# Performance work log

Hardware: AMD Instinct MI355X
Metric: run time of the kernel (lower is better)

## Reference

```python
import jax, jax.numpy as jnp
import numpy as np

ROPE_BASE = 10000.0
WINDOW = 1024  # per_layer_sliding_window
SCALE = 0.08838834764831845  # 1/sqrt(128)
NEG_INF = -1e30


def _apply_rope(x, positions):
    # x: [B, S, H, D]; positions: [B, S] int
    D = x.shape[-1]
    inv_freq = 1.0 / (ROPE_BASE ** (jnp.arange(0, D, 2, dtype=jnp.float32) / D))  # [D/2]
    ang = positions.astype(jnp.float32)[..., None] * inv_freq          # [B, S, D/2]
    cos = jnp.cos(ang)[:, :, None, :]                                   # [B, S, 1, D/2]
    sin = jnp.sin(ang)[:, :, None, :]
    x1, x2 = x[..., : D // 2], x[..., D // 2 :]
    return jnp.concatenate([x1 * cos - x2 * sin, x2 * cos + x1 * sin], axis=-1)


def setup_inputs() -> dict:
    key = jax.random.key(0)
    k1, k2, k3, k4 = jax.random.split(key, 4)
    B, S, H, KV, D = 1, 2048, 32, 8, 128
    q = jax.random.normal(k1, (B, S, H, D), dtype=jnp.float32)
    k = jax.random.normal(k2, (B, S, KV, D), dtype=jnp.float32)
    v = jax.random.normal(k3, (B, S, KV, D), dtype=jnp.float32)
    positions = jnp.broadcast_to(jnp.arange(S, dtype=jnp.int32), (B, S))
    sinks = jax.random.normal(k4, (H,), dtype=jnp.float32)
    return {"q": q, "k": k, "v": v, "positions": positions, "sinks": sinks}


def reference(q, k, v, positions, sinks):
    # q: [B,S,H,D]; k,v: [B,S,KV,D]; positions: [B,S]; sinks: [H]
    B, S, H, D = q.shape
    KV = k.shape[2]
    group = H // KV

    qr = _apply_rope(q, positions)
    kr = _apply_rope(k, positions)

    # GQA: expand kv heads to match q heads
    kr = jnp.repeat(kr, group, axis=2)  # [B,S,H,D]
    ve = jnp.repeat(v, group, axis=2)   # [B,S,H,D]

    scores = jnp.einsum("bqhd,bkhd->bhqk", qr, kr) * SCALE  # [B,H,Q,K]

    pq = positions[:, :, None]  # [B,Q,1]
    pk = positions[:, None, :]  # [B,1,K]
    allowed = (pk <= pq) & (pq - pk < WINDOW)               # causal + sliding window
    scores = jnp.where(allowed[:, None, :, :], scores, NEG_INF)

    # softmax with per-head attention sink logit in the denominator
    sink = sinks[None, :, None]                             # [1,H,1]
    m = jnp.maximum(jnp.max(scores, axis=-1), sink)         # [B,H,Q]
    p = jnp.exp(scores - m[..., None])                      # [B,H,Q,K]
    denom = jnp.sum(p, axis=-1) + jnp.exp(sink - m)         # [B,H,Q]
    out = jnp.einsum("bhqk,bkhd->bqhd", p, ve) / denom.transpose(0, 2, 1)[..., None]
    return out  # [B,S,H,D]
```

## Files before the change

### kernel.cpp

```cpp
#include <hip/hip_runtime.h>

#define S_LEN 2048
#define NH 32
#define NKV 8
#define HD 128
#define WINDOW 1024
#define SCALEF 0.08838834764831845f
#define NEG_INF_F -1e30f
#define NEG_L2_10K_O64 -0.2076205059304601f
#define LOG2E 1.442695040888963f
#define CSHIFT_L2 17.31234049067355f

typedef unsigned short ushort_t;
typedef __attribute__((ext_vector_type(8))) short short8;
typedef __attribute__((ext_vector_type(4))) float floatx4;
typedef __attribute__((ext_vector_type(4))) int intx4;

static __device__ __forceinline__ float fexp2(float x) {
  return __builtin_amdgcn_exp2f(x);
}

static __device__ __forceinline__ ushort_t f2bf(float f) {
  union { float f; unsigned u; } un; un.f = f;
  unsigned r = un.u + 0x7fffu + ((un.u >> 16) & 1u);
  return (ushort_t)(r >> 16);
}

static __device__ __forceinline__ unsigned pack2bf(float a, float b) {
  return (unsigned)f2bf(a) | ((unsigned)f2bf(b) << 16);
}

__device__ __forceinline__ void gl_lds16(const ushort_t* g, ushort_t* l) {
  __builtin_amdgcn_global_load_lds(
      (const __attribute__((address_space(1))) unsigned int*)g,
      (__attribute__((address_space(3))) unsigned int*)l, 16, 0, 0);
}

__global__ __launch_bounds__(256) void prep_kv(
    const float* __restrict__ k, const float* __restrict__ v,
    const int* __restrict__ positions, ushort_t* __restrict__ Kr,
    ushort_t* __restrict__ Vt) {
  __shared__ float lv[64][129];
  const int kv = blockIdx.x & 7;
  const int s0 = (blockIdx.x >> 3) * 64;
  const int tid = threadIdx.x;

  {
    const int i = tid & 63;
    const int wrow = tid >> 6;
    const float invf = fexp2((float)i * NEG_L2_10K_O64);
#pragma unroll 4
    for (int it = 0; it < 16; ++it) {
      int s = s0 + it * 4 + wrow;
      float pos = (float)positions[s];
      const float* kp = k + ((size_t)s * NKV + kv) * HD;
      float x1 = kp[i], x2 = kp[i + 64];
      float sn, cs;
      __sincosf(pos * invf, &sn, &cs);
      ushort_t* o = Kr + ((size_t)kv * S_LEN + s) * HD;
      o[i] = f2bf(x1 * cs - x2 * sn);
      o[i + 64] = f2bf(x2 * cs + x1 * sn);
    }
  }
  {
    const int d = tid & 127;
    const int r2 = tid >> 7;
#pragma unroll
    for (int it = 0; it < 32; ++it) {
      int row = it * 2 + r2;
      lv[row][d] = v[((size_t)(s0 + row) * NKV + kv) * HD + d];
    }
  }
  __syncthreads();
  {
    const int ss = tid & 63;
    const int d0 = tid >> 6;
#pragma unroll
    for (int it = 0; it < 32; ++it) {
      int d = d0 + it * 4;
      Vt[((size_t)kv * HD + d) * S_LEN + s0 + ss] = f2bf(lv[ss][d]);
    }
  }
}

__global__ __launch_bounds__(256, 4) void attn_kernel(
    const float* __restrict__ q, const int* __restrict__ positions,
    const float* __restrict__ sinks, const ushort_t* __restrict__ Kr,
    const ushort_t* __restrict__ Vt, float* __restrict__ out) {
  __shared__ __align__(16) ushort_t smem[16384];

  const int tid = threadIdx.x;
  const int w = tid >> 6;
  const int lane = tid & 63;
  const int quad = lane >> 4;
  const int l16 = lane & 15;
  const int kv = blockIdx.x & 7;
  const int tile = blockIdx.x >> 3;
  const int h = kv * 4 + w;
  const int q0 = tile * 16;

  ushort_t* Qsw = smem + w * 2048;
  {
    const float invf = fexp2((float)lane * NEG_L2_10K_O64);
#pragma unroll 4
    for (int row = 0; row < 16; ++row) {
      float pos = (float)positions[q0 + row];
      const float* qp = q + ((size_t)(q0 + row) * NH + h) * HD;
      float x1 = qp[lane], x2 = qp[lane + 64];
      float sn, cs;
      __sincosf(pos * invf, &sn, &cs);
      float o1 = (x1 * cs - x2 * sn) * SCALEF;
      float o2 = (x2 * cs + x1 * sn) * SCALEF;
      int c1_ = (lane >> 3) ^ row;
      int c2_ = ((lane >> 3) + 8) ^ row;
      Qsw[row * 128 + c1_ * 8 + (lane & 7)] = f2bf(o1);
      Qsw[row * 128 + c2_ * 8 + (lane & 7)] = f2bf(o2);
    }
  }
  short8 qf[4];
#pragma unroll
  for (int t = 0; t < 4; ++t)
    qf[t] = *(const short8*)&Qsw[l16 * 128 + (((4 * t + quad) ^ l16) * 8)];
  __syncthreads();

  const ushort_t* KrH = Kr + (size_t)kv * S_LEN * HD;
  const ushort_t* VtH = Vt + (size_t)kv * HD * S_LEN;
  int kgo[2], vgo[2], ldst[2];
#pragma unroll
  for (int i = 0; i < 2; ++i) {
    int slot = i * 256 + tid;
    int key = slot >> 4;
    int cin = (slot & 15) ^ (key & 15);
    kgo[i] = key * HD + cin * 8;
    int d = slot >> 2;
    int qcin = (slot & 3) ^ ((d ^ (d >> 2)) & 3);
    vgo[i] = d * S_LEN + qcin * 8;
    ldst[i] = (i * 256 + (tid & 192)) * 8;
  }

  auto stage = [&](int b, int koff) {
#pragma unroll
    for (int i = 0; i < 2; ++i) {
      gl_lds16(KrH + (size_t)koff * HD + kgo[i], smem + b * 4096 + ldst[i]);
      gl_lds16(VtH + koff + vgo[i], smem + 8192 + b * 4096 + ldst[i]);
    }
  };

  floatx4 O4[8];
#pragma unroll
  for (int i = 0; i < 8; ++i) O4[i] = (floatx4){0.f, 0.f, 0.f, 0.f};
  float lsum = 0.f;

  const int cbeg = (q0 > 1023) ? ((q0 - 1023) >> 5) : 0;
  const int cend = (q0 + 15) >> 5;

  stage(0, cbeg * 32);
  __syncthreads();

  for (int ci = cbeg; ci <= cend; ++ci) {
    const int b = (ci - cbeg) & 1;
    const int koff = ci * 32;
    if (ci < cend) stage(b ^ 1, koff + 32);

    const ushort_t* KsB = smem + b * 4096;
    const ushort_t* VsB = smem + 8192 + b * 4096;

    floatx4 s0v = (floatx4){0.f, 0.f, 0.f, 0.f};
    floatx4 s1v = (floatx4){0.f, 0.f, 0.f, 0.f};
#pragma unroll
    for (int t = 0; t < 4; ++t) {
      int ch = ((4 * t + quad) ^ l16) * 8;
      short8 k0 = *(const short8*)&KsB[l16 * 128 + ch];
      short8 k1 = *(const short8*)&KsB[(l16 + 16) * 128 + ch];
      s0v = __builtin_amdgcn_mfma_f32_16x16x32_bf16(k0, qf[t], s0v, 0, 0, 0);
      s1v = __builtin_amdgcn_mfma_f32_16x16x32_bf16(k1, qf[t], s1v, 0, 0, 0);
    }

    if (koff + 31 > q0 || koff < q0 - 1008) {
      const int qp_ = q0 + l16;
#pragma unroll
      for (int r = 0; r < 4; ++r) {
        int k0i = koff + quad * 4 + r, k1i = k0i + 16;
        if (!((k0i <= qp_) && (qp_ - k0i < WINDOW))) s0v[r] = NEG_INF_F;
        if (!((k1i <= qp_) && (qp_ - k1i < WINDOW))) s1v[r] = NEG_INF_F;
      }
    }

    float pc0[4], pc1[4];
#pragma unroll
    for (int r = 0; r < 4; ++r) {
      pc0[r] = fexp2(fmaf(s0v[r], LOG2E, -CSHIFT_L2));
      pc1[r] = fexp2(fmaf(s1v[r], LOG2E, -CSHIFT_L2));
    }
    lsum += (pc0[0] + pc0[1]) + (pc0[2] + pc0[3]) +
            (pc1[0] + pc1[1]) + (pc1[2] + pc1[3]);

    unsigned pk0[2] = {pack2bf(pc0[0], pc0[1]), pack2bf(pc0[2], pc0[3])};
    unsigned pk1[2] = {pack2bf(pc1[0], pc1[1]), pack2bf(pc1[2], pc1[3])};
    intx4 bi;
    const int sbase = ((quad & 1) * 2) * 16 + l16;
#pragma unroll
    for (int u = 0; u < 4; ++u) {
      int src = sbase + (u >> 1) * 16;
      int lo = __shfl((int)pk0[u & 1], src);
      int hi = __shfl((int)pk1[u & 1], src);
      bi[u] = (quad < 2) ? lo : hi;
    }
    short8 pb = __builtin_bit_cast(short8, bi);

#pragma unroll
    for (int i = 0; i < 8; ++i) {
      int d = 16 * i + l16;
      short8 vf = *(const short8*)&VsB[d * 32 + ((quad ^ ((d ^ (d >> 2)) & 3)) * 8)];
      O4[i] = __builtin_amdgcn_mfma_f32_16x16x32_bf16(vf, pb, O4[i], 0, 0, 0);
    }

    __syncthreads();
  }

  lsum += __shfl_xor(lsum, 16);
  lsum += __shfl_xor(lsum, 32);
  lsum += fexp2(fmaf(sinks[h], LOG2E, -CSHIFT_L2));
  const float rl = 1.0f / lsum;

  float* op = out + ((size_t)(q0 + l16) * NH + h) * HD;
#pragma unroll
  for (int i = 0; i < 8; ++i) {
    floatx4 val = O4[i] * rl;
    *(floatx4*)(op + 16 * i + quad * 4) = val;
  }
}

extern "C" void kernel_launch(void* const* d_in, const int* in_sizes, int n_in,
                              void* d_out, int out_size, void* d_ws, size_t ws_size,
                              hipStream_t stream) {
  const float* q = (const float*)d_in[0];
  const float* k = (const float*)d_in[1];
  const float* v = (const float*)d_in[2];
  const int* positions = (const int*)d_in[3];
  const float* sinks = (const float*)d_in[4];
  float* out = (float*)d_out;

  ushort_t* Kr = (ushort_t*)d_ws;
  ushort_t* Vt = Kr + (size_t)NKV * S_LEN * HD;

  prep_kv<<<NKV * (S_LEN / 64), 256, 0, stream>>>(k, v, positions, Kr, Vt);
  attn_kernel<<<NKV * (S_LEN / 16), 256, 0, stream>>>(q, positions, sinks, Kr, Vt, out);
}
```

Before: 148.5 us.

## Rewrite attention with 32x32 MFMA, fragment-ordered K/V layout, and split-K waves

The K and V preprocessing now writes rotated K and transposed V straight into MFMA fragment order, so the attention kernel loads operands from global memory into registers and no longer stages them through LDS. Each block handles two query heads per wave pair using 32x32x16 bf16 MFMA. The key chunks are split across two waves and their partial results are merged through LDS at the end. Query tiles are paired, one early and one late, to balance causal work across blocks, and the fixed exp shift is removed in favour of folding log2e into the Q scale. The risks are overflow, since exp is no longer shifted, more register pressure, and more global load latency without double buffering.

```diff
diff --git a/kernel.cpp b/kernel.cpp
--- a/kernel.cpp
+++ b/kernel.cpp
@@ -5,15 +5,14 @@
 #define NKV 8
 #define HD 128
 #define WINDOW 1024
-#define SCALEF 0.08838834764831845f
 #define NEG_INF_F -1e30f
 #define NEG_L2_10K_O64 -0.2076205059304601f
-#define LOG2E 1.442695040888963f
-#define CSHIFT_L2 17.31234049067355f
+#define LOG2E_F 1.442695040888963f
 
 typedef unsigned short ushort_t;
 typedef __attribute__((ext_vector_type(8))) short short8;
 typedef __attribute__((ext_vector_type(4))) float floatx4;
+typedef __attribute__((ext_vector_type(16))) float floatx16;
 typedef __attribute__((ext_vector_type(4))) int intx4;
 
 static __device__ __forceinline__ float fexp2(float x) {
@@ -26,21 +25,17 @@
   return (ushort_t)(r >> 16);
 }
 
-static __device__ __forceinline__ unsigned pack2bf(float a, float b) {
-  return (unsigned)f2bf(a) | ((unsigned)f2bf(b) << 16);
-}
-
-__device__ __forceinline__ void gl_lds16(const ushort_t* g, ushort_t* l) {
-  __builtin_amdgcn_global_load_lds(
-      (const __attribute__((address_space(1))) unsigned int*)g,
-      (__attribute__((address_space(3))) unsigned int*)l, 16, 0, 0);
+static __device__ __forceinline__ unsigned packP(float a, float b) {
+  unsigned ua = __builtin_bit_cast(unsigned, a) + 0x8000u;
+  unsigned ub = __builtin_bit_cast(unsigned, b) + 0x8000u;
+  return __builtin_amdgcn_perm(ub, ua, 0x07060302u);
 }
 
 __global__ __launch_bounds__(256) void prep_kv(
     const float* __restrict__ k, const float* __restrict__ v,
-    const int* __restrict__ positions, ushort_t* __restrict__ Kr,
-    ushort_t* __restrict__ Vt) {
-  __shared__ float lv[64][129];
+    const int* __restrict__ positions, ushort_t* __restrict__ Kr2,
+    ushort_t* __restrict__ Vt2) {
+  __shared__ __align__(16) ushort_t lt[64 * 136];
   const int kv = blockIdx.x & 7;
   const int s0 = (blockIdx.x >> 3) * 64;
   const int tid = threadIdx.x;
@@ -51,183 +46,218 @@
     const float invf = fexp2((float)i * NEG_L2_10K_O64);
 #pragma unroll 4
     for (int it = 0; it < 16; ++it) {
-      int s = s0 + it * 4 + wrow;
+      int row = it * 4 + wrow;
+      int s = s0 + row;
       float pos = (float)positions[s];
       const float* kp = k + ((size_t)s * NKV + kv) * HD;
       float x1 = kp[i], x2 = kp[i + 64];
       float sn, cs;
       __sincosf(pos * invf, &sn, &cs);
-      ushort_t* o = Kr + ((size_t)kv * S_LEN + s) * HD;
-      o[i] = f2bf(x1 * cs - x2 * sn);
-      o[i + 64] = f2bf(x2 * cs + x1 * sn);
-    }
-  }
+      lt[row * 136 + i] = f2bf(x1 * cs - x2 * sn);
+      lt[row * 136 + i + 64] = f2bf(x2 * cs + x1 * sn);
+    }
+  }
+  __syncthreads();
+#pragma unroll
+  for (int it = 0; it < 4; ++it) {
+    int slot = it * 256 + tid;
+    int kb_l = slot >> 9;
+    int rem = slot & 511;
+    int t = rem >> 6;
+    int lane = rem & 63;
+    int key_l = kb_l * 32 + (lane & 31);
+    int dbase = t * 16 + (lane >> 5) * 8;
+    short8 val = *(const short8*)&lt[key_l * 136 + dbase];
+    *(short8*)&Kr2[(size_t)(kv * 64 + (s0 >> 5) + kb_l) * 4096 + t * 512 + lane * 8] = val;
+  }
+  __syncthreads();
   {
     const int d = tid & 127;
     const int r2 = tid >> 7;
 #pragma unroll
     for (int it = 0; it < 32; ++it) {
       int row = it * 2 + r2;
-      lv[row][d] = v[((size_t)(s0 + row) * NKV + kv) * HD + d];
+      lt[row * 136 + d] = f2bf(v[((size_t)(s0 + row) * NKV + kv) * HD + d]);
     }
   }
   __syncthreads();
-  {
-    const int ss = tid & 63;
-    const int d0 = tid >> 6;
-#pragma unroll
-    for (int it = 0; it < 32; ++it) {
-      int d = d0 + it * 4;
-      Vt[((size_t)kv * HD + d) * S_LEN + s0 + ss] = f2bf(lv[ss][d]);
-    }
-  }
-}
-
-__global__ __launch_bounds__(256, 4) void attn_kernel(
+#pragma unroll
+  for (int it = 0; it < 4; ++it) {
+    int slot = it * 256 + tid;
+    int kh_l = slot >> 8;
+    int rem = slot & 255;
+    int tl = rem >> 6;
+    int lane = rem & 63;
+    int d = tl * 32 + (lane & 31);
+    int key0 = kh_l * 16 + (lane >> 5) * 8;
+    unsigned w0 = (unsigned)lt[(key0 + 0) * 136 + d] | ((unsigned)lt[(key0 + 1) * 136 + d] << 16);
+    unsigned w1 = (unsigned)lt[(key0 + 2) * 136 + d] | ((unsigned)lt[(key0 + 3) * 136 + d] << 16);
+    unsigned w2 = (unsigned)lt[(key0 + 4) * 136 + d] | ((unsigned)lt[(key0 + 5) * 136 + d] << 16);
+    unsigned w3 = (unsigned)lt[(key0 + 6) * 136 + d] | ((unsigned)lt[(key0 + 7) * 136 + d] << 16);
+    intx4 val = {(int)w0, (int)w1, (int)w2, (int)w3};
+    *(intx4*)&Vt2[(size_t)(kv * 128 + (s0 >> 4) + kh_l) * 2048 + tl * 512 + lane * 8] = val;
+  }
+}
+
+__global__ __launch_bounds__(256, 3) void attn_kernel(
     const float* __restrict__ q, const int* __restrict__ positions,
-    const float* __restrict__ sinks, const ushort_t* __restrict__ Kr,
-    const ushort_t* __restrict__ Vt, float* __restrict__ out) {
-  __shared__ __align__(16) ushort_t smem[16384];
+    const float* __restrict__ sinks, const ushort_t* __restrict__ Kr2,
+    const ushort_t* __restrict__ Vt2, float* __restrict__ out) {
+  __shared__ __align__(16) ushort_t smem[20480];
+  __shared__ float lsx[64];
 
   const int tid = threadIdx.x;
   const int w = tid >> 6;
   const int lane = tid & 63;
-  const int quad = lane >> 4;
-  const int l16 = lane & 15;
+  const int u = lane >> 5;
+  const int l15 = lane & 15;
+  const int hp = w & 1;
+  const int kw = w >> 1;
   const int kv = blockIdx.x & 7;
-  const int tile = blockIdx.x >> 3;
-  const int h = kv * 4 + w;
-  const int q0 = tile * 16;
-
-  ushort_t* Qsw = smem + w * 2048;
-  {
-    const float invf = fexp2((float)lane * NEG_L2_10K_O64);
+  const int bid = blockIdx.x >> 3;
+  const int h = kv * 4 + hp * 2 + ((lane >> 4) & 1);
+  const float QSCALE = (float)(0.08838834764831845 * 1.4426950408889634);
+
+  const ushort_t* KbL = Kr2 + (size_t)kv * 64 * 4096 + lane * 8;
+  const ushort_t* VbL = Vt2 + (size_t)kv * 128 * 2048 + lane * 8;
+
+  int tiles[2];
+  int ntiles;
+  if (bid < 64) { tiles[0] = bid + 64; tiles[1] = 0; ntiles = 1; }
+  else          { tiles[0] = bid - 64; tiles[1] = 127 - bid; ntiles = 2; }
+
+  for (int ti = 0; ti < ntiles; ++ti) {
+    const int q0 = tiles[ti] * 16;
+
+    {
+      const int hh = w;
+      const int rbase = (hh >> 1) * 4096;
+      const int i = lane;
+      const float invf = fexp2((float)i * NEG_L2_10K_O64);
+      const int t1 = i >> 4;
+      const int j = i & 7;
+      const int lhalf = ((i >> 3) & 1) * 32 + (hh & 1) * 16;
 #pragma unroll 4
-    for (int row = 0; row < 16; ++row) {
-      float pos = (float)positions[q0 + row];
-      const float* qp = q + ((size_t)(q0 + row) * NH + h) * HD;
-      float x1 = qp[lane], x2 = qp[lane + 64];
-      float sn, cs;
-      __sincosf(pos * invf, &sn, &cs);
-      float o1 = (x1 * cs - x2 * sn) * SCALEF;
-      float o2 = (x2 * cs + x1 * sn) * SCALEF;
-      int c1_ = (lane >> 3) ^ row;
-      int c2_ = ((lane >> 3) + 8) ^ row;
-      Qsw[row * 128 + c1_ * 8 + (lane & 7)] = f2bf(o1);
-      Qsw[row * 128 + c2_ * 8 + (lane & 7)] = f2bf(o2);
-    }
-  }
-  short8 qf[4];
-#pragma unroll
-  for (int t = 0; t < 4; ++t)
-    qf[t] = *(const short8*)&Qsw[l16 * 128 + (((4 * t + quad) ^ l16) * 8)];
-  __syncthreads();
-
-  const ushort_t* KrH = Kr + (size_t)kv * S_LEN * HD;
-  const ushort_t* VtH = Vt + (size_t)kv * HD * S_LEN;
-  int kgo[2], vgo[2], ldst[2];
-#pragma unroll
-  for (int i = 0; i < 2; ++i) {
-    int slot = i * 256 + tid;
-    int key = slot >> 4;
-    int cin = (slot & 15) ^ (key & 15);
-    kgo[i] = key * HD + cin * 8;
-    int d = slot >> 2;
-    int qcin = (slot & 3) ^ ((d ^ (d >> 2)) & 3);
-    vgo[i] = d * S_LEN + qcin * 8;
-    ldst[i] = (i * 256 + (tid & 192)) * 8;
-  }
-
-  auto stage = [&](int b, int koff) {
-#pragma unroll
-    for (int i = 0; i < 2; ++i) {
-      gl_lds16(KrH + (size_t)koff * HD + kgo[i], smem + b * 4096 + ldst[i]);
-      gl_lds16(VtH + koff + vgo[i], smem + 8192 + b * 4096 + ldst[i]);
-    }
-  };
-
-  floatx4 O4[8];
-#pragma unroll
-  for (int i = 0; i < 8; ++i) O4[i] = (floatx4){0.f, 0.f, 0.f, 0.f};
-  float lsum = 0.f;
-
-  const int cbeg = (q0 > 1023) ? ((q0 - 1023) >> 5) : 0;
-  const int cend = (q0 + 15) >> 5;
-
-  stage(0, cbeg * 32);
-  __syncthreads();
-
-  for (int ci = cbeg; ci <= cend; ++ci) {
-    const int b = (ci - cbeg) & 1;
-    const int koff = ci * 32;
-    if (ci < cend) stage(b ^ 1, koff + 32);
-
-    const ushort_t* KsB = smem + b * 4096;
-    const ushort_t* VsB = smem + 8192 + b * 4096;
-
-    floatx4 s0v = (floatx4){0.f, 0.f, 0.f, 0.f};
-    floatx4 s1v = (floatx4){0.f, 0.f, 0.f, 0.f};
-#pragma unroll
-    for (int t = 0; t < 4; ++t) {
-      int ch = ((4 * t + quad) ^ l16) * 8;
-      short8 k0 = *(const short8*)&KsB[l16 * 128 + ch];
-      short8 k1 = *(const short8*)&KsB[(l16 + 16) * 128 + ch];
-      s0v = __builtin_amdgcn_mfma_f32_16x16x32_bf16(k0, qf[t], s0v, 0, 0, 0);
-      s1v = __builtin_amdgcn_mfma_f32_16x16x32_bf16(k1, qf[t], s1v, 0, 0, 0);
-    }
-
-    if (koff + 31 > q0 || koff < q0 - 1008) {
-      const int qp_ = q0 + l16;
-#pragma unroll
-      for (int r = 0; r < 4; ++r) {
-        int k0i = koff + quad * 4 + r, k1i = k0i + 16;
-        if (!((k0i <= qp_) && (qp_ - k0i < WINDOW))) s0v[r] = NEG_INF_F;
-        if (!((k1i <= qp_) && (qp_ - k1i < WINDOW))) s1v[r] = NEG_INF_F;
-      }
-    }
-
-    float pc0[4], pc1[4];
-#pragma unroll
-    for (int r = 0; r < 4; ++r) {
-      pc0[r] = fexp2(fmaf(s0v[r], LOG2E, -CSHIFT_L2));
-      pc1[r] = fexp2(fmaf(s1v[r], LOG2E, -CSHIFT_L2));
-    }
-    lsum += (pc0[0] + pc0[1]) + (pc0[2] + pc0[3]) +
-            (pc1[0] + pc1[1]) + (pc1[2] + pc1[3]);
-
-    unsigned pk0[2] = {pack2bf(pc0[0], pc0[1]), pack2bf(pc0[2], pc0[3])};
-    unsigned pk1[2] = {pack2bf(pc1[0], pc1[1]), pack2bf(pc1[2], pc1[3])};
-    intx4 bi;
-    const int sbase = ((quad & 1) * 2) * 16 + l16;
-#pragma unroll
-    for (int u = 0; u < 4; ++u) {
-      int src = sbase + (u >> 1) * 16;
-      int lo = __shfl((int)pk0[u & 1], src);
-      int hi = __shfl((int)pk1[u & 1], src);
-      bi[u] = (quad < 2) ? lo : hi;
-    }
-    short8 pb = __builtin_bit_cast(short8, bi);
-
-#pragma unroll
-    for (int i = 0; i < 8; ++i) {
-      int d = 16 * i + l16;
-      short8 vf = *(const short8*)&VsB[d * 32 + ((quad ^ ((d ^ (d >> 2)) & 3)) * 8)];
-      O4[i] = __builtin_amdgcn_mfma_f32_16x16x32_bf16(vf, pb, O4[i], 0, 0, 0);
-    }
-
-    __syncthreads();
-  }
-
-  lsum += __shfl_xor(lsum, 16);
-  lsum += __shfl_xor(lsum, 32);
-  lsum += fexp2(fmaf(sinks[h], LOG2E, -CSHIFT_L2));
-  const float rl = 1.0f / lsum;
-
-  float* op = out + ((size_t)(q0 + l16) * NH + h) * HD;
-#pragma unroll
-  for (int i = 0; i < 8; ++i) {
-    floatx4 val = O4[i] * rl;
-    *(floatx4*)(op + 16 * i + quad * 4) = val;
+      for (int row = 0; row < 16; ++row) {
+        float pos = (float)positions[q0 + row];
+        const float* qp = q + ((size_t)(q0 + row) * NH + kv * 4 + hh) * HD;
+        float x1 = qp[i], x2 = qp[i + 64];
+        float sn, cs;
+        __sincosf(pos * invf, &sn, &cs);
+        int ldst = rbase + (lhalf + row) * 8 + j;
+        smem[ldst + t1 * 512] = f2bf((x1 * cs - x2 * sn) * QSCALE);
+        smem[ldst + (t1 + 4) * 512] = f2bf((x2 * cs + x1 * sn) * QSCALE);
+      }
+    }
+    __syncthreads();
+
+    floatx16 O[4];
+#pragma unroll
+    for (int i = 0; i < 4; ++i)
+#pragma unroll
+      for (int e = 0; e < 16; ++e) O[i][e] = 0.f;
+    float lsum = 0.f;
+
+    const int cbeg = (q0 > 1023) ? ((q0 - 1023) >> 5) : 0;
+    const int cend = (q0 + 15) >> 5;
+    const ushort_t* Qreg = smem + hp * 4096 + lane * 8;
+    const int qp_ = q0 + l15;
+
+    for (int ci = cbeg + kw; ci <= cend; ci += 2) {
+      const int koff = ci * 32;
+
+      const ushort_t* kfp = KbL + (size_t)ci * 4096;
+      short8 kf[8];
+#pragma unroll
+      for (int t = 0; t < 8; ++t) kf[t] = *(const short8*)(kfp + t * 512);
+
+      floatx16 C;
+#pragma unroll
+      for (int e = 0; e < 16; ++e) C[e] = 0.f;
+#pragma unroll
+      for (int t = 0; t < 8; ++t) {
+        short8 qt = *(const short8*)(Qreg + t * 512);
+        C = __builtin_amdgcn_mfma_f32_32x32x16_bf16(kf[t], qt, C, 0, 0, 0);
+      }
+
+      const ushort_t* vfp = VbL + (size_t)(ci * 2) * 2048;
+      short8 vf[8];
+#pragma unroll
+      for (int tl = 0; tl < 4; ++tl) {
+        vf[tl * 2 + 0] = *(const short8*)(vfp + tl * 512);
+        vf[tl * 2 + 1] = *(const short8*)(vfp + 2048 + tl * 512);
+      }
+
+      if (koff + 31 > q0 || koff < q0 - 1008) {
+#pragma unroll
+        for (int ri = 0; ri < 16; ++ri) {
+          int key = koff + (ri & 3) + 8 * (ri >> 2) + 4 * u;
+          bool ok = (key <= qp_) && (qp_ - key < WINDOW);
+          if (!ok) C[ri] = NEG_INF_F;
+        }
+      }
+
+#pragma unroll
+      for (int ri = 0; ri < 16; ++ri) C[ri] = fexp2(C[ri]);
+      float s0a = (C[0] + C[1]) + (C[2] + C[3]);
+      float s0b = (C[4] + C[5]) + (C[6] + C[7]);
+      float s1a = (C[8] + C[9]) + (C[10] + C[11]);
+      float s1b = (C[12] + C[13]) + (C[14] + C[15]);
+      lsum += (s0a + s0b) + (s1a + s1b);
+
+      unsigned q01 = packP(C[0], C[1]), q23 = packP(C[2], C[3]);
+      unsigned q45 = packP(C[4], C[5]), q67 = packP(C[6], C[7]);
+      unsigned r01 = packP(C[8], C[9]), r23 = packP(C[10], C[11]);
+      unsigned r45 = packP(C[12], C[13]), r67 = packP(C[14], C[15]);
+      unsigned e01 = __shfl_xor((int)q01, 32), e23 = __shfl_xor((int)q23, 32);
+      unsigned e45 = __shfl_xor((int)q45, 32), e67 = __shfl_xor((int)q67, 32);
+      unsigned f01 = __shfl_xor((int)r01, 32), f23 = __shfl_xor((int)r23, 32);
+      unsigned f45 = __shfl_xor((int)r45, 32), f67 = __shfl_xor((int)r67, 32);
+      intx4 b0v = {(int)(u ? e45 : q01), (int)(u ? e67 : q23),
+                   (int)(u ? q45 : e01), (int)(u ? q67 : e23)};
+      intx4 b1v = {(int)(u ? f45 : r01), (int)(u ? f67 : r23),
+                   (int)(u ? r45 : f01), (int)(u ? r67 : f23)};
+      short8 bh0 = __builtin_bit_cast(short8, b0v);
+      short8 bh1 = __builtin_bit_cast(short8, b1v);
+
+#pragma unroll
+      for (int tl = 0; tl < 4; ++tl) {
+        O[tl] = __builtin_amdgcn_mfma_f32_32x32x16_bf16(vf[tl * 2 + 0], bh0, O[tl], 0, 0, 0);
+        O[tl] = __builtin_amdgcn_mfma_f32_32x32x16_bf16(vf[tl * 2 + 1], bh1, O[tl], 0, 0, 0);
+      }
+    }
+
+    __syncthreads();
+
+    lsum += __shfl_xor(lsum, 32);
+    float* Ef = (float*)smem;
+    const int efb = hp * 4352 + lane * 68;
+    if (kw == 1) {
+#pragma unroll
+      for (int tl = 0; tl < 4; ++tl)
+#pragma unroll
+        for (int g = 0; g < 4; ++g)
+          *(floatx4*)&Ef[efb + tl * 16 + g * 4] =
+              (floatx4){O[tl][4 * g], O[tl][4 * g + 1], O[tl][4 * g + 2], O[tl][4 * g + 3]};
+      if (lane < 32) lsx[hp * 32 + lane] = lsum;
+    }
+    __syncthreads();
+    if (kw == 0) {
+      float den = lsum + lsx[hp * 32 + (lane & 31)] + fexp2(sinks[h] * LOG2E_F);
+      float rl = 1.0f / den;
+      float* op = out + ((size_t)(q0 + l15) * NH + h) * HD;
+#pragma unroll
+      for (int tl = 0; tl < 4; ++tl)
+#pragma unroll
+        for (int g = 0; g < 4; ++g) {
+          floatx4 pv = *(const floatx4*)&Ef[efb + tl * 16 + g * 4];
+          floatx4 vv;
+#pragma unroll
+          for (int e = 0; e < 4; ++e) vv[e] = (O[tl][4 * g + e] + pv[e]) * rl;
+          *(floatx4*)(op + tl * 32 + g * 8 + 4 * u) = vv;
+        }
+    }
+    __syncthreads();
   }
 }
 
@@ -241,9 +271,9 @@
   const float* sinks = (const float*)d_in[4];
   float* out = (float*)d_out;
 
-  ushort_t* Kr = (ushort_t*)d_ws;
-  ushort_t* Vt = Kr + (size_t)NKV * S_LEN * HD;
-
-  prep_kv<<<NKV * (S_LEN / 64), 256, 0, stream>>>(k, v, positions, Kr, Vt);
-  attn_kernel<<<NKV * (S_LEN / 16), 256, 0, stream>>>(q, positions, sinks, Kr, Vt, out);
-}
+  ushort_t* Kr2 = (ushort_t*)d_ws;
+  ushort_t* Vt2 = Kr2 + (size_t)NKV * S_LEN * HD;
+
+  prep_kv<<<NKV * (S_LEN / 64), 256, 0, stream>>>(k, v, positions, Kr2, Vt2);
+  attn_kernel<<<NKV * 96, 256, 0, stream>>>(q, positions, sinks, Kr2, Vt2, out);
+}
```

Result: no change. 151.0 us (+1.7%).
